# Performance work log

Hardware: AMD Instinct MI355X
Metric: run time of the kernel (lower is better)

Reference implementation:

```python
import jax, jax.numpy as jnp
import numpy as np

N = 50000
E = 800000
F_IN = 128
HID = 16
HEADS = 8
CLS = 16
NEG_SLOPE = 0.2


def setup_inputs() -> dict:
    key = jax.random.key(0)
    ks = jax.random.split(key, 12)
    x = jax.random.normal(ks[0], (N, F_IN), dtype=jnp.float32)
    edge_index = jax.random.randint(ks[1], (2, E), 0, N, dtype=jnp.int32)
    s = 0.1
    W1 = jax.random.normal(ks[2], (F_IN, HEADS * HID), dtype=jnp.float32) * s
    att_src1 = jax.random.normal(ks[3], (HEADS, HID), dtype=jnp.float32) * s
    att_dst1 = jax.random.normal(ks[4], (HEADS, HID), dtype=jnp.float32) * s
    b1 = jax.random.normal(ks[5], (HEADS * HID,), dtype=jnp.float32) * s
    W2 = jax.random.normal(ks[6], (HEADS * HID, CLS), dtype=jnp.float32) * s
    att_src2 = jax.random.normal(ks[7], (1, CLS), dtype=jnp.float32) * s
    att_dst2 = jax.random.normal(ks[8], (1, CLS), dtype=jnp.float32) * s
    b2 = jax.random.normal(ks[9], (CLS,), dtype=jnp.float32) * s
    return {"x": x, "edge_index": edge_index, "W1": W1, "att_src1": att_src1,
            "att_dst1": att_dst1, "b1": b1, "W2": W2, "att_src2": att_src2,
            "att_dst2": att_dst2, "b2": b2}


def _gat_conv(x, src, dst, W, a_src, a_dst, b, heads, out_ch, concat):
    n = x.shape[0]
    h = (x @ W).reshape(n, heads, out_ch)                     # [N,H,C]
    alpha_src = (h * a_src[None]).sum(-1)                     # [N,H]
    alpha_dst = (h * a_dst[None]).sum(-1)                     # [N,H]
    e = jax.nn.leaky_relu(alpha_src[src] + alpha_dst[dst], NEG_SLOPE)  # [E,H]
    m = jax.lax.stop_gradient(jax.ops.segment_max(e, dst, num_segments=n))
    e = jnp.exp(e - m[dst])
    denom = jax.ops.segment_sum(e, dst, num_segments=n)
    alpha = e / (denom[dst] + 1e-16)                          # [E,H]
    msg = h[src] * alpha[:, :, None]                          # [E,H,C]
    out = jax.ops.segment_sum(msg, dst, num_segments=n)       # [N,H,C]
    out = out.reshape(n, heads * out_ch) if concat else out.mean(axis=1)
    return out + b


def reference(x, edge_index, W1, att_src1, att_dst1, b1, W2, att_src2, att_dst2, b2):
    # PyG GATConv default add_self_loops=True
    loop = jnp.arange(N, dtype=edge_index.dtype)
    src = jnp.concatenate([edge_index[0], loop])
    dst = jnp.concatenate([edge_index[1], loop])
    h = _gat_conv(x, src, dst, W1, att_src1, att_dst1, b1, HEADS, HID, True)
    h = jax.nn.elu(h)
    # dropout inactive (eval mode)
    out = _gat_conv(h, src, dst, W2, att_src2, att_dst2, b2, 1, CLS, False)
    return out
```

## Files before the change

### kernel.cpp

```cpp
#include <hip/hip_runtime.h>
#include <hip/hip_bf16.h>
#include <limits.h>
#include <math.h>

#define N 50000
#define E_ 800000
#define ETOT 850000
#define HH 128
#define HEADS 8
#define HID 16
#define CLS 16
#define NEG 0.2f
#define NB ((N + 255) / 256)
#define GBM 64
#define GEMM_NB ((N + GBM - 1) / GBM)
#define LINK_NB ((ETOT + 255) / 256)
#define A1_NB ((N*HEADS + 255) / 256)

typedef unsigned short u16;
typedef unsigned int   u32;
typedef short s8v __attribute__((ext_vector_type(8)));
typedef float f4v __attribute__((ext_vector_type(4)));

__device__ __forceinline__ u16 f2bu(float f){
  union{float f; u32 i;} c; c.f = f;
  u32 lsb = (c.i >> 16) & 1u;
  c.i += 0x7fffu + lsb;
  return (u16)(c.i >> 16);
}
__device__ __forceinline__ float bu2f(u16 u){
  union{u32 i; float f;} c; c.i = ((u32)u) << 16; return c.f;
}
__device__ __forceinline__ float blo(u32 u){ union{u32 i; float f;} c; c.i = u << 16; return c.f; }
__device__ __forceinline__ float bhi(u32 u){ union{u32 i; float f;} c; c.i = u & 0xffff0000u; return c.f; }

__global__ __launch_bounds__(256) void k_prep(const float* __restrict__ W1,
                                              const float* __restrict__ W2,
                                              u16* __restrict__ wth, u16* __restrict__ wtl,
                                              u16* __restrict__ w2th, u16* __restrict__ w2tl){
  int i = blockIdx.x*256 + threadIdx.x;
  if(i < 128*128){
    int k = i >> 7, c = i & 127;
    float v = W1[i];
    u16 hi = f2bu(v);
    wth[c*128 + k] = hi;
    wtl[c*128 + k] = f2bu(v - bu2f(hi));
  }
  if(i < 128*16){
    int k = i >> 4, c = i & 15;
    float v = W2[i];
    u16 hi = f2bu(v);
    w2th[c*128 + k] = hi;
    w2tl[c*128 + k] = f2bu(v - bu2f(hi));
  }
}

__global__ __launch_bounds__(256) void k_gemm1link(const float* __restrict__ x,
                                                   const u16* __restrict__ wth,
                                                   const u16* __restrict__ wtl,
                                                   u16* __restrict__ h1b,
                                                   const int* __restrict__ ei,
                                                   int* __restrict__ head,
                                                   int* __restrict__ srcv,
                                                   int* __restrict__ nxt){
  __shared__ u16 xh[GBM][40], xl[GBM][40];
  __shared__ u16 wh[128][40], wl[128][40];
  if(blockIdx.x >= GEMM_NB){
    int e = (blockIdx.x - GEMM_NB)*256 + threadIdx.x;
    if(e < ETOT){
      int s, d;
      if(e < E_){ s = ei[e]; d = ei[E_ + e]; } else { s = d = e - E_; }
      int old = atomicExch(&head[d], e);
      srcv[e] = s;
      nxt[e]  = old;
    }
    return;
  }
  int tid  = threadIdx.x;
  int wv   = tid >> 6;
  int lane = tid & 63;
  int row0 = blockIdx.x * GBM;

  f4v acc[4][2];
  #pragma unroll
  for(int t=0;t<4;t++)
    #pragma unroll
    for(int u=0;u<2;u++) acc[t][u] = (f4v){0.f,0.f,0.f,0.f};

  int xr  = tid >> 2;
  int xkq = (tid & 3) * 8;
  int wc  = tid & 127;
  int wq  = (tid >> 7) * 8;
  int xrow = row0 + xr; if(xrow >= N) xrow = N-1;
  const float* xb = x + (size_t)xrow*128 + xkq;
  int fr = lane & 15, fg = lane >> 4;
  int kk = fg*8;

  for(int kc=0; kc<4; kc++){
    int k0 = kc*32;
    float4 v0 = *(const float4*)(xb + k0);
    float4 v1 = *(const float4*)(xb + k0 + 4);
    __syncthreads();
    {
      float vv[8] = {v0.x,v0.y,v0.z,v0.w,v1.x,v1.y,v1.z,v1.w};
      s8v H, L;
      #pragma unroll
      for(int j=0;j<8;j++){
        u16 h_ = f2bu(vv[j]);
        H[j] = (short)h_;
        L[j] = (short)f2bu(vv[j] - bu2f(h_));
      }
      *(s8v*)&xh[xr][xkq] = H;
      *(s8v*)&xl[xr][xkq] = L;
    }
    #pragma unroll
    for(int j=0;j<2;j++){
      int kq = wq + j*16;
      *(s8v*)&wh[wc][kq] = *(const s8v*)&wth[wc*128 + k0 + kq];
      *(s8v*)&wl[wc][kq] = *(const s8v*)&wtl[wc*128 + k0 + kq];
    }
    __syncthreads();
    s8v a_h[4], a_l[4], b_h[2], b_l[2];
    #pragma unroll
    for(int t=0;t<4;t++){
      a_h[t] = *(const s8v*)&xh[t*16 + fr][kk];
      a_l[t] = *(const s8v*)&xl[t*16 + fr][kk];
    }
    #pragma unroll
    for(int u=0;u<2;u++){
      int col = wv*32 + u*16 + fr;
      b_h[u] = *(const s8v*)&wh[col][kk];
      b_l[u] = *(const s8v*)&wl[col][kk];
    }
    #pragma unroll
    for(int t=0;t<4;t++){
      #pragma unroll
      for(int u=0;u<2;u++){
        acc[t][u] = __builtin_amdgcn_mfma_f32_16x16x32_bf16(a_h[t], b_h[u], acc[t][u], 0,0,0);
        acc[t][u] = __builtin_amdgcn_mfma_f32_16x16x32_bf16(a_h[t], b_l[u], acc[t][u], 0,0,0);
        acc[t][u] = __builtin_amdgcn_mfma_f32_16x16x32_bf16(a_l[t], b_h[u], acc[t][u], 0,0,0);
      }
    }
  }
  #pragma unroll
  for(int t=0;t<4;t++){
    #pragma unroll
    for(int j=0;j<4;j++){
      int row = row0 + t*16 + fg*4 + j;
      if(row < N){
        u16* dst = h1b + (size_t)row*128 + wv*32 + fr;
        dst[0]  = f2bu(acc[t][0][j]);
        dst[16] = f2bu(acc[t][1][j]);
      }
    }
  }
}

__global__ __launch_bounds__(256) void k_alphascan1(const u16* __restrict__ h1b,
                                                    const float* __restrict__ Asv,
                                                    const float* __restrict__ Adv,
                                                    float* __restrict__ as1,
                                                    float* __restrict__ ad1,
                                                    const int* __restrict__ head,
                                                    const int* __restrict__ nxt,
                                                    int* __restrict__ deg,
                                                    int* __restrict__ bsum){
  __shared__ int sm[256];
  if(blockIdx.x < NB){
    int t = threadIdx.x;
    int i = blockIdx.x*256 + t;
    int cnt = 0;
    if(i < N){
      int e = head[i];
      while(e >= 0){ cnt++; e = nxt[e]; }
      deg[i] = cnt;
    }
    sm[t] = cnt;
    __syncthreads();
    #pragma unroll
    for(int ofs=128; ofs>0; ofs>>=1){
      if(t < ofs) sm[t] += sm[t+ofs];
      __syncthreads();
    }
    if(t == 0) bsum[blockIdx.x] = sm[0];
    return;
  }
  int id = (blockIdx.x - NB)*256 + threadIdx.x;
  if(id >= N*HEADS) return;
  int i = id >> 3, h = id & 7;
  const uint4* hv = (const uint4*)(h1b + (size_t)i*HH + h*HID);
  uint4 u0 = hv[0], u1 = hv[1];
  float vals[16] = {blo(u0.x),bhi(u0.x),blo(u0.y),bhi(u0.y),
                    blo(u0.z),bhi(u0.z),blo(u0.w),bhi(u0.w),
                    blo(u1.x),bhi(u1.x),blo(u1.y),bhi(u1.y),
                    blo(u1.z),bhi(u1.z),blo(u1.w),bhi(u1.w)};
  float s=0.f, d=0.f;
  #pragma unroll
  for(int j=0;j<16;j++){
    s = fmaf(vals[j], Asv[h*HID+j], s);
    d = fmaf(vals[j], Adv[h*HID+j], d);
  }
  as1[id]=s; ad1[id]=d;
}

__global__ __launch_bounds__(256) void k_scan3walk(const int* __restrict__ deg,
                                                   const int* __restrict__ bsum,
                                                   const int* __restrict__ head,
                                                   const int* __restrict__ srcv,
                                                   const int* __restrict__ nxt,
                                                   int* __restrict__ off,
                                                   int* __restrict__ csr){
  __shared__ int red[256];
  __shared__ int sm[256];
  int t = threadIdx.x;
  red[t] = (t < blockIdx.x) ? bsum[t] : 0;
  __syncthreads();
  #pragma unroll
  for(int ofs=128; ofs>0; ofs>>=1){
    if(t < ofs) red[t] += red[t+ofs];
    __syncthreads();
  }
  int boff = red[0];
  int i = blockIdx.x*256 + t;
  int v0 = (i < N) ? deg[i] : 0;
  sm[t] = v0;
  __syncthreads();
  #pragma unroll
  for(int ofs=1; ofs<256; ofs<<=1){
    int v = sm[t];
    int add = (t >= ofs) ? sm[t-ofs] : 0;
    __syncthreads();
    sm[t] = v + add;
    __syncthreads();
  }
  if(i < N){
    int excl = boff + sm[t] - v0;
    off[i] = excl;
    if(i == N-1) off[N] = excl + v0;
    int e = head[i];
    int pos = excl;
    while(e >= 0){
      csr[pos++] = srcv[e];
      e = nxt[e];
    }
  }
}

#define CH 32
__global__ __launch_bounds__(256) void k_agg1(const int* __restrict__ off,
                                              const int* __restrict__ csr,
                                              const float* __restrict__ as1,
                                              const float* __restrict__ ad1,
                                              const u32* __restrict__ h1w,
                                              const float* __restrict__ b1,
                                              u32* __restrict__ helu_w){
  __shared__ float wsm[4][CH*8];
  __shared__ int   ssm[4][CH];
  int wv   = threadIdx.x >> 6;
  int lane = threadIdx.x & 63;
  int node = blockIdx.x*4 + wv;
  int beg = off[node], end = off[node+1];
  int h  = lane >> 3;
  int hh = lane & 7;
  int el = lane >> 3;
  float advA = ad1[node*8 + hh];
  float den = 0.f, num0 = 0.f, num1 = 0.f;
  float* wsw = wsm[wv];
  int*   ssw = ssm[wv];
  const u32* hp = h1w + lane;
  for(int base = beg; base < end; base += CH){
    int cnt = end - base; if(cnt > CH) cnt = CH;
    #pragma unroll
    for(int k=0;k<CH;k+=8){
      int e = el + k;
      if(e < cnt){
        int s = csr[base+e];
        if(hh == 0) ssw[e] = s;
        float v = as1[s*8+hh] + advA;
        v = v > 0.f ? v : NEG*v;
        wsw[e*8+hh] = __expf(v);
      }
    }
    int e = 0;
    for(; e+8 <= cnt; e += 8){
      int ss[8]; float ww[8]; u32 uu[8];
      #pragma unroll
      for(int j=0;j<8;j++){ ss[j] = ssw[e+j]; ww[j] = wsw[(e+j)*8+h]; }
      #pragma unroll
      for(int j=0;j<8;j++){ uu[j] = hp[(size_t)ss[j]*64]; }
      #pragma unroll
      for(int j=0;j<8;j++){
        den += ww[j];
        num0 = fmaf(ww[j], blo(uu[j]), num0);
        num1 = fmaf(ww[j], bhi(uu[j]), num1);
      }
    }
    for(; e+4 <= cnt; e += 4){
      int ss[4]; float ww[4]; u32 uu[4];
      #pragma unroll
      for(int j=0;j<4;j++){ ss[j] = ssw[e+j]; ww[j] = wsw[(e+j)*8+h]; }
      #pragma unroll
      for(int j=0;j<4;j++){ uu[j] = hp[(size_t)ss[j]*64]; }
      #pragma unroll
      for(int j=0;j<4;j++){
        den += ww[j];
        num0 = fmaf(ww[j], blo(uu[j]), num0);
        num1 = fmaf(ww[j], bhi(uu[j]), num1);
      }
    }
    for(; e < cnt; e++){
      int s = ssw[e];
      float w = wsw[e*8+h];
      u32 u = hp[(size_t)s*64];
      den += w;
      num0 = fmaf(w, blo(u), num0);
      num1 = fmaf(w, bhi(u), num1);
    }
  }
  float2 bb = ((const float2*)b1)[lane];
  float inv = 1.f / (den + 1e-16f);
  float r0 = num0*inv + bb.x;
  float r1 = num1*inv + bb.y;
  r0 = r0 > 0.f ? r0 : expm1f(r0);
  r1 = r1 > 0.f ? r1 : expm1f(r1);
  helu_w[(size_t)node*64 + lane] = (u32)f2bu(r0) | ((u32)f2bu(r1) << 16);
}

__global__ __launch_bounds__(256) void k_gemm2m(const u16* __restrict__ helu,
                                                const u16* __restrict__ w2th,
                                                const u16* __restrict__ w2tl,
                                                const float* __restrict__ Asv,
                                                const float* __restrict__ Adv,
                                                u16* __restrict__ h2b,
                                                float* __restrict__ as2,
                                                float* __restrict__ ad2){
  __shared__ u16 At[4][16][136];
  __shared__ u16 Bh[16][136], Bl[16][136];
  int tid  = threadIdx.x;
  int wv   = tid >> 6;
  int lane = tid & 63;
  int fr = lane & 15, fg = lane >> 4;
  int row0 = blockIdx.x*64 + wv*16;

  {
    int r = tid >> 4, c8 = (tid & 15)*8;
    *(s8v*)&Bh[r][c8] = *(const s8v*)&w2th[r*128 + c8];
    *(s8v*)&Bl[r][c8] = *(const s8v*)&w2tl[r*128 + c8];
  }
  #pragma unroll
  for(int j=0;j<4;j++){
    int rl = j*4 + (lane >> 4);
    int rg = row0 + rl; if(rg >= N) rg = N-1;
    *(s8v*)&At[wv][rl][(lane & 15)*8] = *(const s8v*)&helu[(size_t)rg*128 + (lane & 15)*8];
  }
  __syncthreads();

  f4v acc = (f4v){0.f,0.f,0.f,0.f};
  #pragma unroll
  for(int kc=0; kc<4; kc++){
    int kk = kc*32 + fg*8;
    s8v a  = *(const s8v*)&At[wv][fr][kk];
    s8v bh = *(const s8v*)&Bh[fr][kk];
    s8v bl = *(const s8v*)&Bl[fr][kk];
    acc = __builtin_amdgcn_mfma_f32_16x16x32_bf16(a, bh, acc, 0,0,0);
    acc = __builtin_amdgcn_mfma_f32_16x16x32_bf16(a, bl, acc, 0,0,0);
  }
  float asv = Asv[fr], adv = Adv[fr];
  #pragma unroll
  for(int j=0;j<4;j++){
    int row = row0 + fg*4 + j;
    float ps = acc[j]*asv, pd = acc[j]*adv;
    ps += __shfl_xor(ps,1); ps += __shfl_xor(ps,2); ps += __shfl_xor(ps,4); ps += __shfl_xor(ps,8);
    pd += __shfl_xor(pd,1); pd += __shfl_xor(pd,2); pd += __shfl_xor(pd,4); pd += __shfl_xor(pd,8);
    if(row < N){
      h2b[(size_t)row*16 + fr] = f2bu(acc[j]);
      if(fr == 0){ as2[row] = ps; ad2[row] = pd; }
    }
  }
}

__global__ __launch_bounds__(256) void k_agg2(const int* __restrict__ off,
                                              const int* __restrict__ csr,
                                              const float* __restrict__ as2,
                                              const float* __restrict__ ad2,
                                              const u32* __restrict__ h2w,
                                              const float* __restrict__ b2,
                                              float* __restrict__ outp){
  int t = threadIdx.x;
  int node = blockIdx.x*32 + (t >> 3);
  int c2 = t & 7;
  if(node >= N) return;
  int beg = off[node], end = off[node+1];
  float adv = ad2[node];
  float den = 0.f, num0 = 0.f, num1 = 0.f;
  int gbase = t & 56;
  for(int base = beg; base < end; base += 8){
    int cnt = end - base; if(cnt > 8) cnt = 8;
    float w_my = 0.f; int s_my = 0;
    if(c2 < cnt){
      s_my = csr[base + c2];
      float v = as2[s_my] + adv;
      v = v > 0.f ? v : NEG*v;
      w_my = __expf(v);
    }
    float ww[8]; int ss[8]; u32 uu[8];
    #pragma unroll
    for(int j=0;j<8;j++){
      ww[j] = __shfl(w_my, gbase | j);
      ss[j] = __shfl(s_my, gbase | j);
    }
    #pragma unroll
    for(int j=0;j<8;j++){
      if(j < cnt) uu[j] = h2w[(size_t)ss[j]*8 + c2];
    }
    #pragma unroll
    for(int j=0;j<8;j++){
      if(j < cnt){
        den += ww[j];
        num0 = fmaf(ww[j], blo(uu[j]), num0);
        num1 = fmaf(ww[j], bhi(uu[j]), num1);
      }
    }
  }
  float inv = 1.f / (den + 1e-16f);
  float2 bb = ((const float2*)b2)[c2];
  float2 r;
  r.x = num0*inv + bb.x;
  r.y = num1*inv + bb.y;
  ((float2*)outp)[(size_t)node*8 + c2] = r;
}

extern "C" void kernel_launch(void* const* d_in, const int* in_sizes, int n_in,
                              void* d_out, int out_size, void* d_ws, size_t ws_size,
                              hipStream_t stream){
  const float* x     = (const float*)d_in[0];
  const int*   ei    = (const int*)  d_in[1];
  const float* W1    = (const float*)d_in[2];
  const float* av_s1 = (const float*)d_in[3];
  const float* av_d1 = (const float*)d_in[4];
  const float* b1    = (const float*)d_in[5];
  const float* W2    = (const float*)d_in[6];
  const float* av_s2 = (const float*)d_in[7];
  const float* av_d2 = (const float*)d_in[8];
  const float* b2    = (const float*)d_in[9];
  float* outp = (float*)d_out;

  char* p = (char*)d_ws;
  auto alloc = [&](size_t bytes){ char* q = p; p += (bytes + 255) & ~(size_t)255; return q; };
  u16*   h1b    = (u16*)  alloc((size_t)N*HH*2);
  u16*   helu_b = (u16*)  alloc((size_t)N*HH*2);
  u16*   h2b    = (u16*)  alloc((size_t)N*CLS*2);
  float* as1    = (float*)alloc((size_t)N*HEADS*4);
  float* ad1    = (float*)alloc((size_t)N*HEADS*4);
  float* as2    = (float*)alloc((size_t)N*4);
  float* ad2    = (float*)alloc((size_t)N*4);
  int*   deg    = (int*)  alloc((size_t)N*4);
  int*   head   = (int*)  alloc((size_t)N*4);
  int*   off    = (int*)  alloc((size_t)(N+1)*4);
  int*   csr    = (int*)  alloc((size_t)ETOT*4);
  int*   srcv   = (int*)  alloc((size_t)ETOT*4);
  int*   nxt    = (int*)  alloc((size_t)ETOT*4);
  u16*   wth    = (u16*)  alloc((size_t)128*128*2);
  u16*   wtl    = (u16*)  alloc((size_t)128*128*2);
  u16*   w2th   = (u16*)  alloc((size_t)16*128*2);
  u16*   w2tl   = (u16*)  alloc((size_t)16*128*2);
  int*   bsum   = (int*)  alloc((size_t)NB*4);

  hipMemsetAsync(head, 0xFF, (size_t)N*4, stream);

  k_prep<<<(128*128+255)/256, 256, 0, stream>>>(W1, W2, wth, wtl, w2th, w2tl);

  k_gemm1link<<<GEMM_NB + LINK_NB, 256, 0, stream>>>(x, wth, wtl, h1b, ei, head, srcv, nxt);

  k_alphascan1<<<NB + A1_NB, 256, 0, stream>>>(h1b, av_s1, av_d1, as1, ad1, head, nxt, deg, bsum);

  k_scan3walk<<<NB, 256, 0, stream>>>(deg, bsum, head, srcv, nxt, off, csr);

  k_agg1<<<N/4, 256, 0, stream>>>(off, csr, as1, ad1, (const u32*)h1b, b1, (u32*)helu_b);

  k_gemm2m<<<(N+63)/64, 256, 0, stream>>>(helu_b, w2th, w2tl, av_s2, av_d2, h2b, as2, ad2);
  k_agg2<<<(N+31)/32, 256, 0, stream>>>(off, csr, as2, ad2, (const u32*)h2b, b2, outp);
}
```

Before: 147.8 us.

## Regroup pipeline stages to merge kernels and cut one launch

```diff
diff --git a/kernel.cpp b/kernel.cpp
--- a/kernel.cpp
+++ b/kernel.cpp
@@ -15,6 +15,7 @@
 #define GBM 64
 #define GEMM_NB ((N + GBM - 1) / GBM)
 #define LINK_NB ((ETOT + 255) / 256)
+#define PREP_NB ((128*128 + 255) / 256)
 #define A1_NB ((N*HEADS + 255) / 256)
 
 typedef unsigned short u16;
@@ -34,46 +35,70 @@
 __device__ __forceinline__ float blo(u32 u){ union{u32 i; float f;} c; c.i = u << 16; return c.f; }
 __device__ __forceinline__ float bhi(u32 u){ union{u32 i; float f;} c; c.i = u & 0xffff0000u; return c.f; }
 
-__global__ __launch_bounds__(256) void k_prep(const float* __restrict__ W1,
-                                              const float* __restrict__ W2,
-                                              u16* __restrict__ wth, u16* __restrict__ wtl,
-                                              u16* __restrict__ w2th, u16* __restrict__ w2tl){
-  int i = blockIdx.x*256 + threadIdx.x;
-  if(i < 128*128){
-    int k = i >> 7, c = i & 127;
-    float v = W1[i];
-    u16 hi = f2bu(v);
-    wth[c*128 + k] = hi;
-    wtl[c*128 + k] = f2bu(v - bu2f(hi));
-  }
-  if(i < 128*16){
-    int k = i >> 4, c = i & 15;
-    float v = W2[i];
-    u16 hi = f2bu(v);
-    w2th[c*128 + k] = hi;
-    w2tl[c*128 + k] = f2bu(v - bu2f(hi));
-  }
-}
-
-__global__ __launch_bounds__(256) void k_gemm1link(const float* __restrict__ x,
+__global__ __launch_bounds__(256) void k_linkprep(const int* __restrict__ ei,
+                                                  int* __restrict__ head,
+                                                  int* __restrict__ srcv,
+                                                  int* __restrict__ nxt,
+                                                  const float* __restrict__ W1,
+                                                  const float* __restrict__ W2,
+                                                  u16* __restrict__ wth, u16* __restrict__ wtl,
+                                                  u16* __restrict__ w2th, u16* __restrict__ w2tl){
+  if(blockIdx.x < PREP_NB){
+    int i = blockIdx.x*256 + threadIdx.x;
+    if(i < 128*128){
+      int k = i >> 7, c = i & 127;
+      float v = W1[i];
+      u16 hi = f2bu(v);
+      wth[c*128 + k] = hi;
+      wtl[c*128 + k] = f2bu(v - bu2f(hi));
+    }
+    if(i < 128*16){
+      int k = i >> 4, c = i & 15;
+      float v = W2[i];
+      u16 hi = f2bu(v);
+      w2th[c*128 + k] = hi;
+      w2tl[c*128 + k] = f2bu(v - bu2f(hi));
+    }
+    return;
+  }
+  int e = (blockIdx.x - PREP_NB)*256 + threadIdx.x;
+  if(e >= ETOT) return;
+  int s, d;
+  if(e < E_){ s = ei[e]; d = ei[E_ + e]; } else { s = d = e - E_; }
+  int old = atomicExch(&head[d], e);
+  srcv[e] = s;
+  nxt[e]  = old;
+}
+
+__global__ __launch_bounds__(256) void k_gemm1walk(const float* __restrict__ x,
                                                    const u16* __restrict__ wth,
                                                    const u16* __restrict__ wtl,
                                                    u16* __restrict__ h1b,
-                                                   const int* __restrict__ ei,
-                                                   int* __restrict__ head,
-                                                   int* __restrict__ srcv,
-                                                   int* __restrict__ nxt){
+                                                   const int* __restrict__ head,
+                                                   const int* __restrict__ nxt,
+                                                   int* __restrict__ deg,
+                                                   int* __restrict__ bsum){
   __shared__ u16 xh[GBM][40], xl[GBM][40];
   __shared__ u16 wh[128][40], wl[128][40];
+  __shared__ int sm[256];
   if(blockIdx.x >= GEMM_NB){
-    int e = (blockIdx.x - GEMM_NB)*256 + threadIdx.x;
-    if(e < ETOT){
-      int s, d;
-      if(e < E_){ s = ei[e]; d = ei[E_ + e]; } else { s = d = e - E_; }
-      int old = atomicExch(&head[d], e);
-      srcv[e] = s;
-      nxt[e]  = old;
-    }
+    int b = blockIdx.x - GEMM_NB;
+    int t = threadIdx.x;
+    int i = b*256 + t;
+    int cnt = 0;
+    if(i < N){
+      int e = head[i];
+      while(e >= 0){ cnt++; e = nxt[e]; }
+      deg[i] = cnt;
+    }
+    sm[t] = cnt;
+    __syncthreads();
+    #pragma unroll
+    for(int ofs=128; ofs>0; ofs>>=1){
+      if(t < ofs) sm[t] += sm[t+ofs];
+      __syncthreads();
+    }
+    if(t == 0) bsum[b] = sm[0];
     return;
   }
   int tid  = threadIdx.x;
@@ -156,33 +181,53 @@
   }
 }
 
-__global__ __launch_bounds__(256) void k_alphascan1(const u16* __restrict__ h1b,
+__global__ __launch_bounds__(256) void k_scan3alpha(const int* __restrict__ deg,
+                                                    const int* __restrict__ bsum,
+                                                    const int* __restrict__ head,
+                                                    const int* __restrict__ srcv,
+                                                    const int* __restrict__ nxt,
+                                                    int* __restrict__ off,
+                                                    int* __restrict__ csr,
+                                                    const u16* __restrict__ h1b,
                                                     const float* __restrict__ Asv,
                                                     const float* __restrict__ Adv,
                                                     float* __restrict__ as1,
-                                                    float* __restrict__ ad1,
-                                                    const int* __restrict__ head,
-                                                    const int* __restrict__ nxt,
-                                                    int* __restrict__ deg,
-                                                    int* __restrict__ bsum){
+                                                    float* __restrict__ ad1){
+  __shared__ int red[256];
   __shared__ int sm[256];
   if(blockIdx.x < NB){
     int t = threadIdx.x;
+    red[t] = (t < blockIdx.x) ? bsum[t] : 0;
+    __syncthreads();
+    #pragma unroll
+    for(int ofs=128; ofs>0; ofs>>=1){
+      if(t < ofs) red[t] += red[t+ofs];
+      __syncthreads();
+    }
+    int boff = red[0];
     int i = blockIdx.x*256 + t;
-    int cnt = 0;
+    int v0 = (i < N) ? deg[i] : 0;
+    sm[t] = v0;
+    __syncthreads();
+    #pragma unroll
+    for(int ofs=1; ofs<256; ofs<<=1){
+      int v = sm[t];
+      int add = (t >= ofs) ? sm[t-ofs] : 0;
+      __syncthreads();
+      sm[t] = v + add;
+      __syncthreads();
+    }
     if(i < N){
+      int excl = boff + sm[t] - v0;
+      off[i] = excl;
+      if(i == N-1) off[N] = excl + v0;
       int e = head[i];
-      while(e >= 0){ cnt++; e = nxt[e]; }
-      deg[i] = cnt;
-    }
-    sm[t] = cnt;
-    __syncthreads();
-    #pragma unroll
-    for(int ofs=128; ofs>0; ofs>>=1){
-      if(t < ofs) sm[t] += sm[t+ofs];
-      __syncthreads();
-    }
-    if(t == 0) bsum[blockIdx.x] = sm[0];
+      int pos = excl;
+      while(e >= 0){
+        csr[pos++] = srcv[e];
+        e = nxt[e];
+      }
+    }
     return;
   }
   int id = (blockIdx.x - NB)*256 + threadIdx.x;
@@ -201,49 +246,6 @@
     d = fmaf(vals[j], Adv[h*HID+j], d);
   }
   as1[id]=s; ad1[id]=d;
-}
-
-__global__ __launch_bounds__(256) void k_scan3walk(const int* __restrict__ deg,
-                                                   const int* __restrict__ bsum,
-                                                   const int* __restrict__ head,
-                                                   const int* __restrict__ srcv,
-                                                   const int* __restrict__ nxt,
-                                                   int* __restrict__ off,
-                                                   int* __restrict__ csr){
-  __shared__ int red[256];
-  __shared__ int sm[256];
-  int t = threadIdx.x;
-  red[t] = (t < blockIdx.x) ? bsum[t] : 0;
-  __syncthreads();
-  #pragma unroll
-  for(int ofs=128; ofs>0; ofs>>=1){
-    if(t < ofs) red[t] += red[t+ofs];
-    __syncthreads();
-  }
-  int boff = red[0];
-  int i = blockIdx.x*256 + t;
-  int v0 = (i < N) ? deg[i] : 0;
-  sm[t] = v0;
-  __syncthreads();
-  #pragma unroll
-  for(int ofs=1; ofs<256; ofs<<=1){
-    int v = sm[t];
-    int add = (t >= ofs) ? sm[t-ofs] : 0;
-    __syncthreads();
-    sm[t] = v + add;
-    __syncthreads();
-  }
-  if(i < N){
-    int excl = boff + sm[t] - v0;
-    off[i] = excl;
-    if(i == N-1) off[N] = excl + v0;
-    int e = head[i];
-    int pos = excl;
-    while(e >= 0){
-      csr[pos++] = srcv[e];
-      e = nxt[e];
-    }
-  }
 }
 
 #define CH 32
@@ -278,7 +280,7 @@
         if(hh == 0) ssw[e] = s;
         float v = as1[s*8+hh] + advA;
         v = v > 0.f ? v : NEG*v;
-        wsw[e*8+hh] = __expf(v);
+        wsm[wv][e*8+hh] = __expf(v);
       }
     }
     int e = 0;
@@ -468,13 +470,13 @@
 
   hipMemsetAsync(head, 0xFF, (size_t)N*4, stream);
 
-  k_prep<<<(128*128+255)/256, 256, 0, stream>>>(W1, W2, wth, wtl, w2th, w2tl);
-
-  k_gemm1link<<<GEMM_NB + LINK_NB, 256, 0, stream>>>(x, wth, wtl, h1b, ei, head, srcv, nxt);
-
-  k_alphascan1<<<NB + A1_NB, 256, 0, stream>>>(h1b, av_s1, av_d1, as1, ad1, head, nxt, deg, bsum);
-
-  k_scan3walk<<<NB, 256, 0, stream>>>(deg, bsum, head, srcv, nxt, off, csr);
+  k_linkprep<<<PREP_NB + LINK_NB, 256, 0, stream>>>(ei, head, srcv, nxt,
+                                                    W1, W2, wth, wtl, w2th, w2tl);
+
+  k_gemm1walk<<<GEMM_NB + NB, 256, 0, stream>>>(x, wth, wtl, h1b, head, nxt, deg, bsum);
+
+  k_scan3alpha<<<NB + A1_NB, 256, 0, stream>>>(deg, bsum, head, srcv, nxt, off, csr,
+                                               h1b, av_s1, av_d1, as1, ad1);
 
   k_agg1<<<N/4, 256, 0, stream>>>(off, csr, as1, ad1, (const u32*)h1b, b1, (u32*)helu_b);
 
```

Measured after the change: 149.0 us. Within noise of the previous version (+0.8%).
